# Kernel optimization log

Hardware: AMD Instinct MI355X
Metric: run time of the kernel (lower is better)

Reference implementation:

```python
import jax, jax.numpy as jnp
import numpy as np

B, N, D = 4, 2048, 1024
HEAD_DIMS = 128
NUM_HEADS = 8
PROJ = HEAD_DIMS * NUM_HEADS  # 1024


def setup_inputs() -> dict:
    key = jax.random.key(0)
    ks = jax.random.split(key, 5)
    # Weights stored as (in, out); xavier-normal-like scale
    def xavier(k, fan_in, fan_out):
        std = (2.0 / (fan_in + fan_out)) ** 0.5
        return jax.random.normal(k, (fan_in, fan_out), dtype=jnp.float32) * std
    return {
        "x": jax.random.normal(ks[0], (B, N, D), dtype=jnp.float32),
        "Wq": xavier(ks[1], D, PROJ),
        "Wk": xavier(ks[2], D, PROJ),
        "Wv": xavier(ks[3], D, PROJ),
        "Wo": xavier(ks[4], PROJ, PROJ),
    }


def reference(x, Wq, Wk, Wv, Wo):
    b, n, d = x.shape
    # QKV projections, split into heads: (b, h, n, hd)
    def split_heads(z):
        return z.reshape(b, n, NUM_HEADS, HEAD_DIMS).transpose(0, 2, 1, 3)
    q = split_heads(x @ Wq)
    k = split_heads(x @ Wk)
    v = split_heads(x @ Wv)
    scale = 1.0 / jnp.sqrt(jnp.float32(HEAD_DIMS))
    logits = jnp.einsum("bhqd,bhkd->bhqk", q, k) * scale
    weights = jax.nn.softmax(logits, axis=-1)
    out = jnp.einsum("bhqk,bhkd->bhqd", weights, v)
    out = out.transpose(0, 2, 1, 3).reshape(b, n, PROJ)
    return out @ Wo
```

## Files before the change

kernel.cpp:

```cpp
#include <hip/hip_runtime.h>
#include <hip/hip_bf16.h>


typedef __attribute__((ext_vector_type(8))) short short8;
typedef __attribute__((ext_vector_type(4))) short short4v;
typedef __attribute__((ext_vector_type(4))) float floatx4;
typedef __attribute__((ext_vector_type(8))) _Float16 half8;

#define MFMA_F16(a, b, c) __builtin_amdgcn_mfma_f32_16x16x32_f16( \
    __builtin_bit_cast(half8, (a)), __builtin_bit_cast(half8, (b)), (c), 0, 0, 0)

static constexpr int BATCH  = 4;
static constexpr int NHEADS = 8;
static constexpr int SEQ    = 2048;
static constexpr int HD     = 128;
static constexpr int DMODEL = 1024;
static constexpr int MROWS  = BATCH * SEQ;
static constexpr int NQKV   = 3 * DMODEL;

#define QSCALE2 0.12752283786512624f

static __device__ __forceinline__ short f16bits(float v) {
    return __builtin_bit_cast(short, (_Float16)v);
}

template <typename T>
static __device__ __forceinline__ short8 load8_f16(const T* p) {
    if constexpr (sizeof(T) == 2) {
        return *(const short8*)p;
    } else {
        const float4 f0 = *(const float4*)p;
        const float4 f1 = *(const float4*)(p + 4);
        short8 r;
        r[0] = f16bits(f0.x); r[1] = f16bits(f0.y);
        r[2] = f16bits(f0.z); r[3] = f16bits(f0.w);
        r[4] = f16bits(f1.x); r[5] = f16bits(f1.y);
        r[6] = f16bits(f1.z); r[7] = f16bits(f1.w);
        return r;
    }
}

static __device__ __forceinline__ void storeC(float* C, size_t idx, float v) {
    C[idx] = v;
}
static __device__ __forceinline__ void storeC(_Float16* C, size_t idx, float v) {
    C[idx] = (_Float16)v;
}

static __device__ __forceinline__ void gload16(const short* g, short* l) {
    __builtin_amdgcn_global_load_lds(
        (const __attribute__((address_space(1))) void*)g,
        (__attribute__((address_space(3))) void*)l, 16, 0, 0);
}

__global__ __launch_bounds__(256)
void prep(const float* __restrict__ x, short* __restrict__ xb,
          const float* __restrict__ W0, const float* __restrict__ W1,
          const float* __restrict__ W2, const float* __restrict__ W3,
          short* __restrict__ Wt, int K, int N)
{
    __shared__ short T[32][33];
    const int z = blockIdx.z;
    if (z >= 4) {
        const size_t chunk = ((size_t)(z - 4) * 1024 + blockIdx.y * 32 + blockIdx.x);
        const size_t i = (chunk * 256 + threadIdx.x) * 8;
        *(short8*)&xb[i] = load8_f16(&x[i]);
        return;
    }
    const float* W = (z == 0) ? W0 : (z == 1) ? W1 : (z == 2) ? W2 : W3;
    short* Wtz = Wt + (size_t)z * K * N;

    const int n0 = blockIdx.x * 32, k0 = blockIdx.y * 32;
    const int r = threadIdx.x >> 3, c4 = (threadIdx.x & 7) * 4;

    const float4 v = *(const float4*)&W[(size_t)(k0 + r) * N + n0 + c4];
    T[r][c4 + 0] = f16bits(v.x);
    T[r][c4 + 1] = f16bits(v.y);
    T[r][c4 + 2] = f16bits(v.z);
    T[r][c4 + 3] = f16bits(v.w);
    __syncthreads();

    short4v o;
    o[0] = T[c4 + 0][r]; o[1] = T[c4 + 1][r];
    o[2] = T[c4 + 2][r]; o[3] = T[c4 + 3][r];
    *(short4v*)&Wtz[(size_t)(n0 + r) * K + k0 + c4] = o;
}

__global__ __launch_bounds__(256)
void convx(const float* __restrict__ x, short* __restrict__ xb)
{
    const size_t i = ((size_t)blockIdx.x * 256 + threadIdx.x) * 8;
    *(short8*)&xb[i] = load8_f16(&x[i]);
}

__global__ __launch_bounds__(256)
void transpose_v(const short* __restrict__ V, short* __restrict__ Vt)
{
    __shared__ short T[64][72];
    const int s0 = blockIdx.x * 64;
    const int d0 = blockIdx.y * 64;
    const int bh = blockIdx.z;
    const short* Vi = V  + (size_t)bh * SEQ * HD;
    short*       Vo = Vt + (size_t)bh * HD * SEQ;

    const int r = threadIdx.x >> 3;
    const int c = threadIdx.x & 7;

    *(short8*)&T[r][c * 8]      = *(const short8*)&Vi[(size_t)(s0 + r) * HD + d0 + c * 8];
    *(short8*)&T[r + 32][c * 8] = *(const short8*)&Vi[(size_t)(s0 + r + 32) * HD + d0 + c * 8];
    __syncthreads();

    short8 o0, o1;
    #pragma unroll
    for (int j = 0; j < 8; ++j) {
        o0[j] = T[c * 8 + j][r];
        o1[j] = T[c * 8 + j][r + 32];
    }
    *(short8*)&Vo[(size_t)(d0 + r) * SEQ + s0 + c * 8]      = o0;
    *(short8*)&Vo[(size_t)(d0 + r + 32) * SEQ + s0 + c * 8] = o1;
}

template <typename OutT, bool QKV>
__global__ __launch_bounds__(256)
void gemm128(const short* __restrict__ A, const short* __restrict__ Bt,
             OutT* __restrict__ C, int M, int N, int K, size_t qkvStride)
{
    __shared__ __align__(16) short As[128 * 64];
    __shared__ __align__(16) short Bs[128 * 64];

    const int tid  = threadIdx.x;
    const int lane = tid & 63;
    const int w    = tid >> 6;
    const int quad = lane >> 4;
    const int l16  = lane & 15;

    const int m0 = blockIdx.x * 128;
    const int n0 = blockIdx.y * 128;
    const int wm = (w >> 1) * 64;
    const int wn = (w & 1) * 64;

    floatx4 acc[4][4] = {};

    const int srow   = tid >> 3;
    const int schunk = (tid & 7) ^ (srow & 7);
    const short* aG = A  + (size_t)(m0 + srow) * K + schunk * 8;
    const short* bG = Bt + (size_t)(n0 + srow) * K + schunk * 8;
    short* aL = As + tid * 8;
    short* bL = Bs + tid * 8;

    const int fsw = l16 & 7;

    for (int k0 = 0; k0 < K; k0 += 64) {
        __syncthreads();
        #pragma unroll
        for (int r = 0; r < 4; ++r) {
            gload16(aG + k0 + (size_t)(r * 32) * K, aL + r * 2048);
            gload16(bG + k0 + (size_t)(r * 32) * K, bL + r * 2048);
        }
        __syncthreads();

        #pragma unroll
        for (int kk = 0; kk < 2; ++kk) {
            short8 af[4], bf[4];
            #pragma unroll
            for (int mi = 0; mi < 4; ++mi)
                af[mi] = *(short8*)&As[(wm + mi * 16 + l16) * 64 +
                                       (((kk * 4 + quad) ^ fsw) * 8)];
            #pragma unroll
            for (int ni = 0; ni < 4; ++ni)
                bf[ni] = *(short8*)&Bs[(wn + ni * 16 + l16) * 64 +
                                       (((kk * 4 + quad) ^ fsw) * 8)];

            #pragma unroll
            for (int mi = 0; mi < 4; ++mi)
                #pragma unroll
                for (int ni = 0; ni < 4; ++ni)
                    acc[mi][ni] = MFMA_F16(af[mi], bf[ni], acc[mi][ni]);
        }
    }

    #pragma unroll
    for (int mi = 0; mi < 4; ++mi)
        #pragma unroll
        for (int ni = 0; ni < 4; ++ni)
            #pragma unroll
            for (int r = 0; r < 4; ++r) {
                const int m = m0 + wm + mi * 16 + quad * 4 + r;
                const int n = n0 + wn + ni * 16 + l16;
                float v = acc[mi][ni][r];
                if constexpr (QKV) {
                    const int qkv = n >> 10, rem = n & 1023;
                    const int h = rem >> 7, d = rem & 127;
                    const int b = m >> 11, s = m & 2047;
                    if (qkv == 0) v *= QSCALE2;
                    storeC(C, (size_t)qkv * qkvStride +
                              (((size_t)b * NHEADS + h) * SEQ + s) * HD + d, v);
                } else {
                    storeC(C, (size_t)m * N + n, v);
                }
            }
}

__global__ __launch_bounds__(128)
void attn_flash11(const short* __restrict__ Q, const short* __restrict__ K,
                  const short* __restrict__ Vt, _Float16* __restrict__ O)
{
    __shared__ __align__(16) short Ks[2][32 * 128];
    __shared__ __align__(16) short Vs[2][128 * 32];
    __shared__ __align__(16) short Plds[2][32 * 40];

    const int tid  = threadIdx.x;
    const int lane = tid & 63;
    const int w    = tid >> 6;
    const int quad = lane >> 4;
    const int l16  = lane & 15;

    const int h  = blockIdx.x & 7;
    const int qi = blockIdx.x >> 3;
    const int b  = blockIdx.y;
    const int q0 = qi * 64;

    const short* Qh  = Q  + (((size_t)b * NHEADS + h) * SEQ) * HD;
    const short* Kh  = K  + (((size_t)b * NHEADS + h) * SEQ) * HD;
    const short* Vth = Vt + (((size_t)b * NHEADS + h) * HD) * SEQ;

    short8 qf[2][4];
    #pragma unroll
    for (int mi = 0; mi < 2; ++mi) {
        const int qrow = q0 + w * 32 + mi * 16 + l16;
        #pragma unroll
        for (int c = 0; c < 4; ++c)
            qf[mi][c] = *(const short8*)&Qh[(size_t)qrow * HD + c * 32 + quad * 8];
    }

    const int kr0 = tid >> 4, kc0 = tid & 15;
    const short* kA0 = Kh + (size_t)kr0 * HD + ((kc0 ^ kr0) * 8);
    const short* kA1 = Kh + (size_t)(kr0 + 8) * HD + ((kc0 ^ (kr0 + 8)) * 8);
    const int vr0 = tid >> 2, vp0 = tid & 3;
    const short* vA = Vth + (size_t)vr0 * SEQ + ((vp0 ^ ((vr0 >> 1) & 3)) * 8);

    floatx4 acc[2][8] = {};
    floatx4 acc9[2] = {};

    short8 ones;
    #pragma unroll
    for (int j = 0; j < 8; ++j) ones[j] = 0x3C00;

    const int fswV = (l16 >> 1) & 3;
    short* Pw = &Plds[w][0];

    auto STAGE = [&](short* kDst, short* vDst, int tile) {
        const size_t ko = (size_t)tile * 32 * HD;
        const size_t vo = (size_t)tile * 32;
        gload16(kA0 + ko,            kDst + tid * 8);
        gload16(kA1 + ko,            kDst + (tid + 128) * 8);
        gload16(kA0 + ko + 16 * HD,  kDst + (tid + 256) * 8);
        gload16(kA1 + ko + 16 * HD,  kDst + (tid + 384) * 8);
        gload16(vA + vo,                        vDst + tid * 8);
        gload16(vA + vo + (size_t)32 * SEQ,     vDst + (tid + 128) * 8);
        gload16(vA + vo + (size_t)64 * SEQ,     vDst + (tid + 256) * 8);
        gload16(vA + vo + (size_t)96 * SEQ,     vDst + (tid + 384) * 8);
    };

    auto COMPUTE = [&](const short* Kb, const short* Vb) {
        floatx4 s[2][2] = {};
        #pragma unroll
        for (int c = 0; c < 4; ++c) {
            const int k_ = c * 4 + quad;
            short8 kf0 = *(short8*)&Kb[l16 * 128 + ((k_ ^ l16) * 8)];
            short8 kf1 = *(short8*)&Kb[(16 + l16) * 128 + ((k_ ^ l16) * 8)];
            #pragma unroll
            for (int mi = 0; mi < 2; ++mi) {
                s[mi][0] = MFMA_F16(qf[mi][c], kf0, s[mi][0]);
                s[mi][1] = MFMA_F16(qf[mi][c], kf1, s[mi][1]);
            }
        }
        #pragma unroll
        for (int mi = 0; mi < 2; ++mi)
            #pragma unroll
            for (int r = 0; r < 4; ++r) {
                const float p0 = __builtin_amdgcn_exp2f(s[mi][0][r]);
                const float p1 = __builtin_amdgcn_exp2f(s[mi][1][r]);
                const int prow = mi * 16 + quad * 4 + r;
                Pw[prow * 40 + l16]      = f16bits(p0);
                Pw[prow * 40 + 16 + l16] = f16bits(p1);
            }
        short8 pf[2];
        #pragma unroll
        for (int mi = 0; mi < 2; ++mi) {
            pf[mi] = *(short8*)&Pw[(mi * 16 + l16) * 40 + quad * 8];
            acc9[mi] = MFMA_F16(pf[mi], ones, acc9[mi]);
        }
        #pragma unroll
        for (int hc = 0; hc < 8; ++hc) {
            short8 vf = *(short8*)&Vb[(hc * 16 + l16) * 32 + ((quad ^ fswV) * 8)];
            #pragma unroll
            for (int mi = 0; mi < 2; ++mi)
                acc[mi][hc] = MFMA_F16(pf[mi], vf, acc[mi][hc]);
        }
    };

    STAGE(&Ks[0][0], &Vs[0][0], 0);

    for (int kt = 0; kt < SEQ; kt += 64) {
        const int t = kt >> 5;
        __syncthreads();
        STAGE(&Ks[1][0], &Vs[1][0], t + 1);
        COMPUTE(&Ks[0][0], &Vs[0][0]);
        __syncthreads();
        if (kt + 64 < SEQ)
            STAGE(&Ks[0][0], &Vs[0][0], t + 2);
        COMPUTE(&Ks[1][0], &Vs[1][0]);
    }

    #pragma unroll
    for (int mi = 0; mi < 2; ++mi) {
        float rinv[4];
        #pragma unroll
        for (int r = 0; r < 4; ++r)
            rinv[r] = 1.0f / fmaxf(acc9[mi][r], 1e-30f);
        #pragma unroll
        for (int hc = 0; hc < 8; ++hc)
            #pragma unroll
            for (int r = 0; r < 4; ++r) {
                const int row = q0 + w * 32 + mi * 16 + quad * 4 + r;
                O[((size_t)b * SEQ + row) * DMODEL + h * HD + hc * 16 + l16] =
                    (_Float16)(acc[mi][hc][r] * rinv[r]);
            }
    }
}

template <typename AT, typename OutT>
__global__ __launch_bounds__(256)
void gemm64(const AT* __restrict__ A, const float* __restrict__ W,
            OutT* __restrict__ C, int M, int N, int K, int headsplit)
{
    __shared__ __align__(16) short As[64][32];
    __shared__ __align__(16) short Bs[64][32];

    const int tid  = threadIdx.x;
    const int lane = tid & 63;
    const int w    = tid >> 6;
    const int quad = lane >> 4;
    const int l16  = lane & 15;

    const int m0 = blockIdx.x * 64;
    const int n0 = blockIdx.y * 64;
    const int wm = (w >> 1) * 32;
    const int wn = (w & 1) * 32;

    floatx4 acc[2][2] = {};

    const int arow = tid >> 2, acol = (tid & 3) * 8;
    const int brow = tid >> 3, bcol = (tid & 7) * 8;

    const AT*    aptr = A + (size_t)(m0 + arow) * K + acol;
    const float* bptr = W + (size_t)brow * N + n0 + bcol;

    for (int k0 = 0; k0 < K; k0 += 32) {
        short8 av = load8_f16(aptr + k0);
        short8 bv = load8_f16(bptr + (size_t)k0 * N);
        __syncthreads();
        *(short8*)&As[arow][acol] = av;
        #pragma unroll
        for (int j = 0; j < 8; ++j)
            Bs[bcol + j][brow] = bv[j];
        __syncthreads();

        short8 af0 = *(short8*)&As[wm + l16][quad * 8];
        short8 af1 = *(short8*)&As[wm + 16 + l16][quad * 8];
        short8 bf0 = *(short8*)&Bs[wn + l16][quad * 8];
        short8 bf1 = *(short8*)&Bs[wn + 16 + l16][quad * 8];

        acc[0][0] = MFMA_F16(af0, bf0, acc[0][0]);
        acc[0][1] = MFMA_F16(af0, bf1, acc[0][1]);
        acc[1][0] = MFMA_F16(af1, bf0, acc[1][0]);
        acc[1][1] = MFMA_F16(af1, bf1, acc[1][1]);
    }

    #pragma unroll
    for (int mi = 0; mi < 2; ++mi)
        #pragma unroll
        for (int ni = 0; ni < 2; ++ni)
            #pragma unroll
            for (int r = 0; r < 4; ++r) {
                const int m = m0 + wm + mi * 16 + quad * 4 + r;
                const int n = n0 + wn + ni * 16 + l16;
                const float v = acc[mi][ni][r];
                if (headsplit) {
                    const int b = m >> 11, nn = m & 2047;
                    const int h = n >> 7,  d  = n & 127;
                    storeC(C, (((size_t)b * NHEADS + h) * SEQ + nn) * HD + d, v);
                } else {
                    storeC(C, (size_t)m * N + n, v);
                }
            }
}

__global__ __launch_bounds__(256)
void attn_flash(const short* __restrict__ Q, const short* __restrict__ K,
                const short* __restrict__ V, _Float16* __restrict__ O)
{
    __shared__ __align__(16) short Ksf[32][136];
    __shared__ __align__(16) short Vtl[HD][40];
    __shared__ __align__(16) short Pldsf[4][16][40];

    const int tid  = threadIdx.x;
    const int lane = tid & 63;
    const int w    = tid >> 6;
    const int quad = lane >> 4;
    const int l16  = lane & 15;

    const int q0 = blockIdx.x * 64;
    const int h  = blockIdx.y;
    const int b  = blockIdx.z;

    const size_t headoff = ((size_t)b * NHEADS + h) * SEQ * HD;
    const short* Qh = Q + headoff;
    const short* Kh = K + headoff;
    const short* Vh = V + headoff;

    const float scale = 0.08838834764831845f;

    const int qrow = q0 + w * 16 + l16;
    short8 qf[4];
    #pragma unroll
    for (int c = 0; c < 4; ++c)
        qf[c] = *(const short8*)&Qh[(size_t)qrow * HD + c * 32 + quad * 8];

    float mrow[4], lrow[4];
    #pragma unroll
    for (int r = 0; r < 4; ++r) { mrow[r] = -1e30f; lrow[r] = 0.f; }
    floatx4 acc[8] = {};

    const int krow = tid >> 4, kcol = (tid & 15) * 8;
    const int vkey = tid & 31;
    const int vhd  = (tid >> 5) * 16;

    for (int kt = 0; kt < SEQ; kt += 32) {
        const short* Kt = Kh + (size_t)kt * HD;
        short8 k0v = *(const short8*)(Kt + (size_t)tid * 8);
        short8 k1v = *(const short8*)(Kt + (size_t)(tid + 256) * 8);
        short8 v0 = *(const short8*)&Vh[(size_t)(kt + vkey) * HD + vhd];
        short8 v1 = *(const short8*)&Vh[(size_t)(kt + vkey) * HD + vhd + 8];

        __syncthreads();
        *(short8*)&Ksf[krow][kcol]      = k0v;
        *(short8*)&Ksf[krow + 16][kcol] = k1v;
        #pragma unroll
        for (int j = 0; j < 8; ++j) {
            Vtl[vhd + j][vkey]     = v0[j];
            Vtl[vhd + 8 + j][vkey] = v1[j];
        }
        __syncthreads();

        floatx4 s0 = {}, s1 = {};
        #pragma unroll
        for (int c = 0; c < 4; ++c) {
            short8 kf0 = *(short8*)&Ksf[l16][c * 32 + quad * 8];
            short8 kf1 = *(short8*)&Ksf[16 + l16][c * 32 + quad * 8];
            s0 = MFMA_F16(qf[c], kf0, s0);
            s1 = MFMA_F16(qf[c], kf1, s1);
        }

        float p0[4], p1[4], alpha[4];
        #pragma unroll
        for (int r = 0; r < 4; ++r) {
            const float a  = s0[r] * scale;
            const float bb = s1[r] * scale;
            float mx = fmaxf(a, bb);
            mx = fmaxf(mx, __shfl_xor(mx, 1));
            mx = fmaxf(mx, __shfl_xor(mx, 2));
            mx = fmaxf(mx, __shfl_xor(mx, 4));
            mx = fmaxf(mx, __shfl_xor(mx, 8));
            const float mnew = fmaxf(mrow[r], mx);
            alpha[r] = __expf(mrow[r] - mnew);
            mrow[r]  = mnew;
            p0[r] = __expf(a - mnew);
            p1[r] = __expf(bb - mnew);
            float rs = p0[r] + p1[r];
            rs += __shfl_xor(rs, 1);
            rs += __shfl_xor(rs, 2);
            rs += __shfl_xor(rs, 4);
            rs += __shfl_xor(rs, 8);
            lrow[r] = lrow[r] * alpha[r] + rs;
        }
        #pragma unroll
        for (int hc = 0; hc < 8; ++hc)
            #pragma unroll
            for (int r = 0; r < 4; ++r)
                acc[hc][r] *= alpha[r];

        #pragma unroll
        for (int r = 0; r < 4; ++r) {
            Pldsf[w][quad * 4 + r][l16]      = f16bits(p0[r]);
            Pldsf[w][quad * 4 + r][16 + l16] = f16bits(p1[r]);
        }
        __syncthreads();

        short8 pf = *(short8*)&Pldsf[w][l16][quad * 8];
        #pragma unroll
        for (int hc = 0; hc < 8; ++hc) {
            short8 vf = *(short8*)&Vtl[hc * 16 + l16][quad * 8];
            acc[hc] = MFMA_F16(pf, vf, acc[hc]);
        }
    }

    #pragma unroll
    for (int hc = 0; hc < 8; ++hc)
        #pragma unroll
        for (int r = 0; r < 4; ++r) {
            const int row = q0 + w * 16 + quad * 4 + r;
            const float val = acc[hc][r] / fmaxf(lrow[r], 1e-30f);
            O[((size_t)b * SEQ + row) * DMODEL + h * HD + hc * 16 + l16] =
                (_Float16)val;
        }
}

extern "C" void kernel_launch(void* const* d_in, const int* in_sizes, int n_in,
                              void* d_out, int out_size, void* d_ws, size_t ws_size,
                              hipStream_t stream)
{
    const float* x  = (const float*)d_in[0];
    const float* Wq = (const float*)d_in[1];
    const float* Wk = (const float*)d_in[2];
    const float* Wv = (const float*)d_in[3];
    const float* Wo = (const float*)d_in[4];
    float* out = (float*)d_out;

    const size_t bufElems = (size_t)MROWS * DMODEL;
    const size_t batElems = (size_t)SEQ * DMODEL;
    const size_t MiB = 1024 * 1024;
    dim3 tt(256);
    dim3 ta(128);

    if (ws_size >= 72 * MiB) {
        short* xb    = (short*)d_ws;
        short* Qb    = xb + bufElems;
        short* Kb    = xb + 2 * bufElems;
        short* Vn    = xb + 3 * bufElems;
        short* Wtall = xb + 4 * bufElems;
        short* Wto   = Wtall + 3 * (size_t)DMODEL * DMODEL;
        short* VtG   = xb;
        short* Ab    = Vn;

        prep<<<dim3(32, 32, 8), tt, 0, stream>>>(
            x, xb, Wq, Wk, Wv, Wo, Wtall, DMODEL, DMODEL);

        gemm128<_Float16, true><<<dim3(MROWS / 128, NQKV / 128), tt, 0, stream>>>(
            xb, Wtall, (_Float16*)Qb, MROWS, NQKV, DMODEL, bufElems);

        transpose_v<<<dim3(SEQ / 64, HD / 64, BATCH * NHEADS), tt, 0, stream>>>(Vn, VtG);

        attn_flash11<<<dim3(NHEADS * (SEQ / 64), BATCH), ta, 0, stream>>>(
            Qb, Kb, VtG, (_Float16*)Ab);

        gemm128<float, false><<<dim3(MROWS / 128, DMODEL / 128), tt, 0, stream>>>(
            Ab, Wto, out, MROWS, DMODEL, DMODEL, 0);
    } else if (ws_size >= 64 * MiB) {
        short* xb    = (short*)d_ws;
        short* Qb    = xb + 2 * batElems;
        short* Kb    = Qb + 4 * batElems;
        short* Vn    = Kb + 4 * batElems;
        short* Wtall = Vn + 4 * batElems;
        short* Wto   = Wtall + 3 * (size_t)DMODEL * DMODEL;

        prep<<<dim3(32, 32, 4), tt, 0, stream>>>(
            nullptr, nullptr, Wq, Wk, Wv, Wo, Wtall, DMODEL, DMODEL);

        for (int half = 0; half < 2; ++half) {
            const size_t off = (size_t)half * 2 * batElems;
            convx<<<dim3(2048), tt, 0, stream>>>(x + off, xb);
            gemm128<_Float16, true><<<dim3(32, NQKV / 128), tt, 0, stream>>>(
                xb, Wtall, (_Float16*)(Qb + off), 2 * SEQ, NQKV, DMODEL,
                4 * batElems);
        }
        for (int half = 0; half < 2; ++half) {
            const size_t off = (size_t)half * 2 * batElems;
            transpose_v<<<dim3(SEQ / 64, HD / 64, 2 * NHEADS), tt, 0, stream>>>(
                Vn + off, xb);
            attn_flash11<<<dim3(NHEADS * (SEQ / 64), 2), ta, 0, stream>>>(
                Qb + off, Kb + off, xb, (_Float16*)(Vn + off));
        }
        gemm128<float, false><<<dim3(MROWS / 128, DMODEL / 128), tt, 0, stream>>>(
            Vn, Wto, out, MROWS, DMODEL, DMODEL, 0);
    } else if (ws_size >= 24 * MiB) {
        short* xb    = (short*)d_ws;
        short* Qb    = xb + batElems;
        short* Kb    = xb + 2 * batElems;
        short* Vb    = xb + 3 * batElems;
        short* Wtall = xb + 4 * batElems;
        short* Wto   = Wtall + 3 * (size_t)DMODEL * DMODEL;

        prep<<<dim3(32, 32, 4), tt, 0, stream>>>(
            nullptr, nullptr, Wq, Wk, Wv, Wo, Wtall, DMODEL, DMODEL);

        for (int b = 0; b < BATCH; ++b) {
            convx<<<dim3(1024), tt, 0, stream>>>(x + (size_t)b * batElems, xb);
            gemm128<_Float16, true><<<dim3(SEQ / 128, NQKV / 128), tt, 0, stream>>>(
                xb, Wtall, (_Float16*)Qb, SEQ, NQKV, DMODEL, batElems);
            transpose_v<<<dim3(SEQ / 64, HD / 64, NHEADS), tt, 0, stream>>>(Vb, xb);
            attn_flash11<<<dim3(NHEADS * (SEQ / 64), 1), ta, 0, stream>>>(
                Qb, Kb, xb, (_Float16*)Vb);
            gemm128<float, false><<<dim3(SEQ / 128, DMODEL / 128), tt, 0, stream>>>(
                Vb, Wto, out + (size_t)b * batElems, SEQ, DMODEL, DMODEL, 0);
        }
    } else {
        short* Qb = (short*)d_ws;
        short* Kb = Qb + batElems;
        short* Vb = Qb + 2 * batElems;
        short* Ab = Qb + 3 * batElems;

        dim3 gg(SEQ / 64, DMODEL / 64);
        for (int b = 0; b < BATCH; ++b) {
            const float* xb_ = x + (size_t)b * batElems;
            gemm64<float, _Float16><<<gg, tt, 0, stream>>>(
                xb_, Wq, (_Float16*)Qb, SEQ, DMODEL, DMODEL, 1);
            gemm64<float, _Float16><<<gg, tt, 0, stream>>>(
                xb_, Wk, (_Float16*)Kb, SEQ, DMODEL, DMODEL, 1);
            gemm64<float, _Float16><<<gg, tt, 0, stream>>>(
                xb_, Wv, (_Float16*)Vb, SEQ, DMODEL, DMODEL, 1);
            attn_flash<<<dim3(SEQ / 64, NHEADS, 1), tt, 0, stream>>>(
                Qb, Kb, Vb, (_Float16*)Ab);
            gemm64<short, float><<<gg, tt, 0, stream>>>(
                Ab, Wo, out + (size_t)b * batElems, SEQ, DMODEL, DMODEL, 0);
        }
    }
}
```

Before: 291.3 us.

## Software-pipeline attention: overlap next tile's QK with current exp and PV

Splits the K and V staging and restructures the attention loop so the QK^T MFMAs for tile t+1 are issued while exp and P·V of tile t run. K is prefetched two tiles ahead and V one tile ahead, and there is now one barrier per tile instead of two per pair. The aim is to hide the exp/LDS latency of the softmax step behind matrix-core work. The cost is an extra set of score registers, which raises register pressure and could lower occupancy.

After: 292.3 us. About the same (+0.3%).

```diff
diff --git a/kernel.cpp b/kernel.cpp
--- a/kernel.cpp
+++ b/kernel.cpp
@@ -202,7 +202,7 @@
 }
 
 __global__ __launch_bounds__(128)
-void attn_flash11(const short* __restrict__ Q, const short* __restrict__ K,
+void attn_flash12(const short* __restrict__ Q, const short* __restrict__ K,
                   const short* __restrict__ Vt, _Float16* __restrict__ O)
 {
     __shared__ __align__(16) short Ks[2][32 * 128];
@@ -249,21 +249,22 @@
     const int fswV = (l16 >> 1) & 3;
     short* Pw = &Plds[w][0];
 
-    auto STAGE = [&](short* kDst, short* vDst, int tile) {
+    auto STAGE_K = [&](short* dst, int tile) {
         const size_t ko = (size_t)tile * 32 * HD;
+        gload16(kA0 + ko,           dst + tid * 8);
+        gload16(kA1 + ko,           dst + (tid + 128) * 8);
+        gload16(kA0 + ko + 16 * HD, dst + (tid + 256) * 8);
+        gload16(kA1 + ko + 16 * HD, dst + (tid + 384) * 8);
+    };
+    auto STAGE_V = [&](short* dst, int tile) {
         const size_t vo = (size_t)tile * 32;
-        gload16(kA0 + ko,            kDst + tid * 8);
-        gload16(kA1 + ko,            kDst + (tid + 128) * 8);
-        gload16(kA0 + ko + 16 * HD,  kDst + (tid + 256) * 8);
-        gload16(kA1 + ko + 16 * HD,  kDst + (tid + 384) * 8);
-        gload16(vA + vo,                        vDst + tid * 8);
-        gload16(vA + vo + (size_t)32 * SEQ,     vDst + (tid + 128) * 8);
-        gload16(vA + vo + (size_t)64 * SEQ,     vDst + (tid + 256) * 8);
-        gload16(vA + vo + (size_t)96 * SEQ,     vDst + (tid + 384) * 8);
+        gload16(vA + vo,                      dst + tid * 8);
+        gload16(vA + vo + (size_t)32 * SEQ,   dst + (tid + 128) * 8);
+        gload16(vA + vo + (size_t)64 * SEQ,   dst + (tid + 256) * 8);
+        gload16(vA + vo + (size_t)96 * SEQ,   dst + (tid + 384) * 8);
     };
 
-    auto COMPUTE = [&](const short* Kb, const short* Vb) {
-        floatx4 s[2][2] = {};
+    auto QK = [&](const short* Kb, floatx4 (&s)[2][2]) {
         #pragma unroll
         for (int c = 0; c < 4; ++c) {
             const int k_ = c * 4 + quad;
@@ -275,22 +276,38 @@
                 s[mi][1] = MFMA_F16(qf[mi][c], kf1, s[mi][1]);
             }
         }
+    };
+
+    auto ITER = [&](int T, int BB, floatx4 (&sin)[2][2], floatx4 (&sout)[2][2]) {
+        __syncthreads();
+        if (T + 2 < SEQ / 32) STAGE_K(&Ks[BB][0], T + 2);
+        if (T + 1 < SEQ / 32) STAGE_V(&Vs[BB ^ 1][0], T + 1);
+
         #pragma unroll
         for (int mi = 0; mi < 2; ++mi)
             #pragma unroll
             for (int r = 0; r < 4; ++r) {
-                const float p0 = __builtin_amdgcn_exp2f(s[mi][0][r]);
-                const float p1 = __builtin_amdgcn_exp2f(s[mi][1][r]);
+                const float p0 = __builtin_amdgcn_exp2f(sin[mi][0][r]);
+                const float p1 = __builtin_amdgcn_exp2f(sin[mi][1][r]);
                 const int prow = mi * 16 + quad * 4 + r;
                 Pw[prow * 40 + l16]      = f16bits(p0);
                 Pw[prow * 40 + 16 + l16] = f16bits(p1);
             }
+
+        #pragma unroll
+        for (int mi = 0; mi < 2; ++mi) {
+            sout[mi][0] = floatx4{};
+            sout[mi][1] = floatx4{};
+        }
+        if (T + 1 < SEQ / 32) QK(&Ks[BB ^ 1][0], sout);
+
         short8 pf[2];
         #pragma unroll
         for (int mi = 0; mi < 2; ++mi) {
             pf[mi] = *(short8*)&Pw[(mi * 16 + l16) * 40 + quad * 8];
             acc9[mi] = MFMA_F16(pf[mi], ones, acc9[mi]);
         }
+        const short* Vb = &Vs[BB][0];
         #pragma unroll
         for (int hc = 0; hc < 8; ++hc) {
             short8 vf = *(short8*)&Vb[(hc * 16 + l16) * 32 + ((quad ^ fswV) * 8)];
@@ -300,17 +317,16 @@
         }
     };
 
-    STAGE(&Ks[0][0], &Vs[0][0], 0);
-
-    for (int kt = 0; kt < SEQ; kt += 64) {
-        const int t = kt >> 5;
-        __syncthreads();
-        STAGE(&Ks[1][0], &Vs[1][0], t + 1);
-        COMPUTE(&Ks[0][0], &Vs[0][0]);
-        __syncthreads();
-        if (kt + 64 < SEQ)
-            STAGE(&Ks[0][0], &Vs[0][0], t + 2);
-        COMPUTE(&Ks[1][0], &Vs[1][0]);
+    STAGE_K(&Ks[0][0], 0);
+    STAGE_V(&Vs[0][0], 0);
+    STAGE_K(&Ks[1][0], 1);
+    __syncthreads();
+    floatx4 sc[2][2] = {}, sn[2][2];
+    QK(&Ks[0][0], sc);
+
+    for (int t = 0; t < SEQ / 32; t += 2) {
+        ITER(t,     0, sc, sn);
+        ITER(t + 1, 1, sn, sc);
     }
 
     #pragma unroll
@@ -552,7 +568,7 @@
 
         transpose_v<<<dim3(SEQ / 64, HD / 64, BATCH * NHEADS), tt, 0, stream>>>(Vn, VtG);
 
-        attn_flash11<<<dim3(NHEADS * (SEQ / 64), BATCH), ta, 0, stream>>>(
+        attn_flash12<<<dim3(NHEADS * (SEQ / 64), BATCH), ta, 0, stream>>>(
             Qb, Kb, VtG, (_Float16*)Ab);
 
         gemm128<float, false><<<dim3(MROWS / 128, DMODEL / 128), tt, 0, stream>>>(
@@ -579,7 +595,7 @@
             const size_t off = (size_t)half * 2 * batElems;
             transpose_v<<<dim3(SEQ / 64, HD / 64, 2 * NHEADS), tt, 0, stream>>>(
                 Vn + off, xb);
-            attn_flash11<<<dim3(NHEADS * (SEQ / 64), 2), ta, 0, stream>>>(
+            attn_flash12<<<dim3(NHEADS * (SEQ / 64), 2), ta, 0, stream>>>(
                 Qb + off, Kb + off, xb, (_Float16*)(Vn + off));
         }
         gemm128<float, false><<<dim3(MROWS / 128, DMODEL / 128), tt, 0, stream>>>(
@@ -600,7 +616,7 @@
             gemm128<_Float16, true><<<dim3(SEQ / 128, NQKV / 128), tt, 0, stream>>>(
                 xb, Wtall, (_Float16*)Qb, SEQ, NQKV, DMODEL, batElems);
             transpose_v<<<dim3(SEQ / 64, HD / 64, NHEADS), tt, 0, stream>>>(Vb, xb);
-            attn_flash11<<<dim3(NHEADS * (SEQ / 64), 1), ta, 0, stream>>>(
+            attn_flash12<<<dim3(NHEADS * (SEQ / 64), 1), ta, 0, stream>>>(
                 Qb, Kb, xb, (_Float16*)Vb);
             gemm128<float, false><<<dim3(SEQ / 128, DMODEL / 128), tt, 0, stream>>>(
                 Vb, Wto, out + (size_t)b * batElems, SEQ, DMODEL, DMODEL, 0);
```
